# Performance work log

Hardware: AMD Instinct MI355X
Metric: run time of the kernel (lower is better)

## Reference

```python
import jax, jax.numpy as jnp
import numpy as np

N = 384      # max_nodes
H = 256      # layers[0] == layers[1] == layers[2]
Z = 128      # dim_z
ED = 128     # edge_dim
AH = ED // 2 # attention hidden

# complete directed graph: combinations (i<j) then reversed pairs
_i, _j = np.triu_indices(N, k=1)
_SRC = jnp.asarray(np.concatenate([_i, _j]), dtype=jnp.int32)  # edge_index[0]
_DST = jnp.asarray(np.concatenate([_j, _i]), dtype=jnp.int32)  # edge_index[1]


def setup_inputs() -> dict:
    key = jax.random.key(0)
    ks = jax.random.split(key, 16)
    def p(k, shape, fan_in):
        return jax.random.normal(k, shape, dtype=jnp.float32) * (1.0 / np.sqrt(fan_in))
    return {
        "z": jax.random.normal(ks[0], (1, Z), dtype=jnp.float32),
        # GRU (torch layout: W_ih [3H, Z], W_hh [3H, H]; gate order r, z, n)
        "gru_Wih": p(ks[1], (3 * H, Z), Z),
        "gru_Whh": p(ks[2], (3 * H, H), H),
        "gru_bih": jnp.zeros((3 * H,), jnp.float32),
        "gru_bhh": jnp.zeros((3 * H,), jnp.float32),
        # edge_generator MLP: 2H -> 4H -> ED
        "eg_W1": p(ks[3], (2 * H, 4 * H), 2 * H), "eg_b1": jnp.zeros((4 * H,), jnp.float32),
        "eg_W2": p(ks[4], (4 * H, ED), 4 * H),   "eg_b2": jnp.zeros((ED,), jnp.float32),
        # attention MLPs: (ED+H) -> ED//2 -> 1
        "att0_W1": p(ks[5], (ED + H, AH), ED + H), "att0_b1": jnp.zeros((AH,), jnp.float32),
        "att0_W2": p(ks[6], (AH, 1), AH),           "att0_b2": jnp.zeros((1,), jnp.float32),
        "att1_W1": p(ks[7], (ED + H, AH), ED + H), "att1_b1": jnp.zeros((AH,), jnp.float32),
        "att1_W2": p(ks[8], (AH, 1), AH),           "att1_b2": jnp.zeros((1,), jnp.float32),
        # EdgeConv output linears: H -> H
        "conv0_W": p(ks[9], (H, H), H),  "conv0_b": jnp.zeros((H,), jnp.float32),
        "conv1_W": p(ks[10], (H, H), H), "conv1_b": jnp.zeros((H,), jnp.float32),
    }


def _forward(z, gru_Wih, gru_Whh, gru_bih, gru_bhh,
             eg_W1, eg_b1, eg_W2, eg_b2,
             att0_W1, att0_b1, att0_W2, att0_b2,
             att1_W1, att1_b1, att1_W2, att1_b2,
             conv0_W, conv0_b, conv1_W, conv1_b):
    # --- GRU node generation: input is the same latent z at every step ---
    gi = z[0] @ gru_Wih.T + gru_bih            # [3H], constant per step
    gir, giz, gin = jnp.split(gi, 3)
    def step(h, _):
        gh = h @ gru_Whh.T + gru_bhh
        ghr, ghz, ghn = jnp.split(gh, 3)
        r = jax.nn.sigmoid(gir + ghr)
        u = jax.nn.sigmoid(giz + ghz)
        n = jnp.tanh(gin + r * ghn)
        h2 = (1.0 - u) * n + u * h
        return h2, h2
    _, nodes = jax.lax.scan(step, jnp.zeros((H,), z.dtype), None, length=N)  # [N, H]

    # --- edge features over the complete directed graph ---
    pairs = jnp.concatenate([nodes[_SRC], nodes[_DST]], axis=-1)            # [E, 2H]
    edges = jax.nn.relu(pairs @ eg_W1 + eg_b1) @ eg_W2 + eg_b2              # [E, ED]

    # --- EdgeConv: gather src, attention MLP gate, scatter-sum, linear ---
    def conv(x, aW1, ab1, aW2, ab2, W, b):
        xs = x[_SRC]                                                        # [E, H]
        a_in = jnp.concatenate([edges, xs], axis=-1)                        # [E, ED+H]
        att = jax.nn.sigmoid(jax.nn.relu(a_in @ aW1 + ab1) @ aW2 + ab2)     # [E, 1]
        agg = jax.ops.segment_sum(att * xs, _DST, num_segments=N)           # [N, H]
        return agg @ W + b

    x = jax.nn.relu(conv(nodes, att0_W1, att0_b1, att0_W2, att0_b2, conv0_W, conv0_b))
    x = conv(x, att1_W1, att1_b1, att1_W2, att1_b2, conv1_W, conv1_b)
    return jnp.sum(x, axis=0)                                               # [H]


def reference(z, gru_Wih, gru_Whh, gru_bih, gru_bhh,
              eg_W1, eg_b1, eg_W2, eg_b2,
              att0_W1, att0_b1, att0_W2, att0_b2,
              att1_W1, att1_b1, att1_W2, att1_b2,
              conv0_W, conv0_b, conv1_W, conv1_b):
    return _forward(z, gru_Wih, gru_Whh, gru_bih, gru_bhh,
                    eg_W1, eg_b1, eg_W2, eg_b2,
                    att0_W1, att0_b1, att0_W2, att0_b2,
                    att1_W1, att1_b1, att1_W2, att1_b2,
                    conv0_W, conv0_b, conv1_W, conv1_b)
```

## Files before the change

### kernel.cpp

```cpp
#include <hip/hip_runtime.h>
#include <hip/hip_fp16.h>
#include <cstdint>

#define DEV static __device__ __forceinline__

typedef _Float16 h2v __attribute__((ext_vector_type(2)));
typedef _Float16 half8 __attribute__((ext_vector_type(8)));
typedef float float4v __attribute__((ext_vector_type(4)));

union U32H2 { uint32_t u; _Float16 f[2]; };

DEV uint32_t pack_f2(float a, float b) {
    auto p = __builtin_amdgcn_cvt_pkrtz(a, b);
    return __builtin_bit_cast(uint32_t, p);
}

DEV half8 bc8(uint4 v) { return __builtin_bit_cast(half8, v); }

DEV float sigmoidf_(float x) { return 1.0f / (1.0f + __expf(-x)); }

DEV void gl_lds16(const void* gsrc, void* ldst) {
    __builtin_amdgcn_global_load_lds(
        (const __attribute__((address_space(1))) uint32_t*)gsrc,
        (__attribute__((address_space(3))) uint32_t*)ldst, 16, 0, 0);
}

DEV float pick4(float4v lo, float4v hi, int bsel, int r) {
    float v0 = bsel ? hi[0] : lo[0];
    float v1 = bsel ? hi[1] : lo[1];
    float v2 = bsel ? hi[2] : lo[2];
    float v3 = bsel ? hi[3] : lo[3];
    float x01 = (r & 1) ? v1 : v0;
    float x23 = (r & 1) ? v3 : v2;
    return (r & 2) ? x23 : x01;
}

static const size_t OFF_W16T  = 0;
static const size_t OFF_GI    = 98304;
static const size_t OFF_CC    = 99072;
static const size_t OFF_BF    = 99200;
static const size_t OFF_NODES = 164736;
static const size_t OFF_PF    = 263040;
static const size_t OFF_QF    = 459648;
static const size_t OFF_R0    = 656256;
static const size_t OFF_R1    = 680832;
static const size_t OFF_TT    = 705408;
static const size_t OFF_ATT0  = 10142592;
static const size_t OFF_ATT1  = 10290048;
static const size_t OFF_AGG   = 10437504;
static const size_t OFF_X0    = 10535808;
static const size_t OFF_CS    = 10634112;
static const size_t OFF_V     = 10634496;
static const size_t WS_TOTAL  = 10634752;

__global__ void k_prep_all(const float* __restrict__ Whh, uint32_t* __restrict__ WL,
                           const float* __restrict__ z, const float* __restrict__ Wih,
                           const float* __restrict__ bih, const float* __restrict__ bhh,
                           float* __restrict__ gs,
                           const float* __restrict__ egb2, const float* __restrict__ a0W1,
                           const float* __restrict__ a1W1, float* __restrict__ cc,
                           const float* __restrict__ egW2, uint32_t* __restrict__ BF) {
    int bb = blockIdx.x;
    if (bb < 96) {
        int o4 = bb * 256 + threadIdx.x;
        int c = o4 >> 9, t = o4 & 511;
        int rt = c >> 3, kt = c & 7;
        int lane = t & 63, wv = t >> 6;
        int row = (rt >> 1) * 256 + wv * 32 + ((rt & 1) << 4) + (lane & 15);
        int k0 = kt*32 + (lane >> 4)*8;
        const float* src = Whh + row*256 + k0;
        uint4 o;
        o.x = pack_f2(src[0], src[1]);
        o.y = pack_f2(src[2], src[3]);
        o.z = pack_f2(src[4], src[5]);
        o.w = pack_f2(src[6], src[7]);
        ((uint4*)WL)[o4] = o;
    } else if (bb < 99) {
        int o = (bb - 96) * 256 + threadIdx.x;
        float acc = bih[o];
        if (o < 512) acc += bhh[o];
        for (int i = 0; i < 128; ++i) acc += Wih[o*128 + i] * z[i];
        gs[o] = acc;
    } else if (bb == 99) {
        int t = threadIdx.x;
        if (t < 128) {
            const float* A = (t < 64) ? a0W1 : a1W1;
            int j = t & 63;
            float acc = 0.f;
            for (int i = 0; i < 128; ++i) acc += egb2[i] * A[i*64 + j];
            cc[t] = acc;
        }
    } else {
        int idx = (bb - 100) * 256 + threadIdx.x;
        int k2 = idx >> 7, n = idx & 127;
        const float* A = (n < 64) ? (a0W1 + n) : (a1W1 + (n - 64));
        const float* w0 = egW2 + (2*k2) * 128;
        float a = 0.f, b = 0.f;
        for (int i = 0; i < 128; ++i) {
            float av = A[i*64];
            a += w0[i] * av;
            b += w0[128 + i] * av;
        }
        int kk = k2 >> 4, jgrp = (k2 >> 2) & 3, sub = k2 & 3;
        int lane = jgrp*16 + (n & 15), t = n >> 4;
        BF[((kk*8 + t)*64 + lane)*4 + sub] = pack_f2(a, b);
    }
}

__global__ void __launch_bounds__(512, 2)
k_gru(const float* __restrict__ gs, const float* __restrict__ bhh,
      const uint32_t* __restrict__ WL, float* __restrict__ nodes) {
    int tid = threadIdx.x;
    int lane = tid & 63, wv = tid >> 6;
    int kq = lane >> 4, c = lane & 15;
    __shared__ __align__(16) _Float16 hh16[512];

    uint4 w[48];
    const uint4* wl4 = (const uint4*)WL;
    #pragma unroll
    for (int cc = 0; cc < 48; ++cc) w[cc] = wl4[cc*512 + tid];
    #pragma unroll
    for (int cc = 0; cc < 48; ++cc)
        asm volatile("" : "+a"(w[cc].x), "+a"(w[cc].y), "+a"(w[cc].z), "+a"(w[cc].w));

    const float L2E = 1.44269504088896f;
    int r = c & 3, bsel = (c >> 2) & 1;
    int i_loc = kq*4 + r + bsel*16;
    int gidx = wv*32 + i_loc;
    float pr = -L2E * gs[gidx];
    float pz = -L2E * gs[256 + gidx];
    float gin_l = gs[512 + gidx];
    float bn_l  = bhh[512 + gidx];
    float pn = -2.f * L2E * gin_l;
    bool active = (c < 8);

    float h = 0.f;
    if (tid < 256) ((uint32_t*)hh16)[tid] = 0u;
    __syncthreads();

    const float4v z4 = {0.f, 0.f, 0.f, 0.f};
    int par = 0;
    for (int t = 0; t < 384; ++t) {
        const _Float16* hb = hh16 + par*256 + kq*8;
        uint4 b[8];
        #pragma unroll
        for (int kt = 0; kt < 8; ++kt) b[kt] = *(const uint4*)(hb + kt*32);

        float4v d0, d1, d2, d3, d4, d5;
        d0 = __builtin_amdgcn_mfma_f32_16x16x32_f16(bc8(w[0]),  bc8(b[0]), z4, 0, 0, 0);
        d1 = __builtin_amdgcn_mfma_f32_16x16x32_f16(bc8(w[8]),  bc8(b[0]), z4, 0, 0, 0);
        #pragma unroll
        for (int kt = 1; kt < 8; ++kt) {
            d0 = __builtin_amdgcn_mfma_f32_16x16x32_f16(bc8(w[kt]),    bc8(b[kt]), d0, 0, 0, 0);
            d1 = __builtin_amdgcn_mfma_f32_16x16x32_f16(bc8(w[8+kt]),  bc8(b[kt]), d1, 0, 0, 0);
        }
        float ghr = pick4(d0, d1, bsel, r);
        float er = __builtin_amdgcn_exp2f(__builtin_fmaf(ghr, -L2E, pr));
        float rg = __builtin_amdgcn_rcpf(1.f + er);

        d2 = __builtin_amdgcn_mfma_f32_16x16x32_f16(bc8(w[16]), bc8(b[0]), z4, 0, 0, 0);
        d3 = __builtin_amdgcn_mfma_f32_16x16x32_f16(bc8(w[24]), bc8(b[0]), z4, 0, 0, 0);
        d4 = __builtin_amdgcn_mfma_f32_16x16x32_f16(bc8(w[32]), bc8(b[0]), z4, 0, 0, 0);
        d5 = __builtin_amdgcn_mfma_f32_16x16x32_f16(bc8(w[40]), bc8(b[0]), z4, 0, 0, 0);
        #pragma unroll
        for (int kt = 1; kt < 8; ++kt) {
            d2 = __builtin_amdgcn_mfma_f32_16x16x32_f16(bc8(w[16+kt]), bc8(b[kt]), d2, 0, 0, 0);
            d3 = __builtin_amdgcn_mfma_f32_16x16x32_f16(bc8(w[24+kt]), bc8(b[kt]), d3, 0, 0, 0);
            d4 = __builtin_amdgcn_mfma_f32_16x16x32_f16(bc8(w[32+kt]), bc8(b[kt]), d4, 0, 0, 0);
            d5 = __builtin_amdgcn_mfma_f32_16x16x32_f16(bc8(w[40+kt]), bc8(b[kt]), d5, 0, 0, 0);
        }

        float ghz = pick4(d2, d3, bsel, r);
        float ghn = pick4(d4, d5, bsel, r);
        float eu = __builtin_amdgcn_exp2f(__builtin_fmaf(ghz, -L2E, pz));
        float u  = __builtin_amdgcn_rcpf(1.f + eu);
        float tm = ghn + bn_l;
        float q  = __builtin_fmaf(rg * tm, -2.f * L2E, pn);
        float e2 = __builtin_amdgcn_exp2f(q);
        float nn = __builtin_fmaf(2.f, __builtin_amdgcn_rcpf(1.f + e2), -1.f);
        h = nn + u * (h - nn);

        if (active) {
            hh16[(par ^ 1)*256 + gidx] = (_Float16)h;
            nodes[t*256 + gidx] = h;
        }
        asm volatile("s_waitcnt lgkmcnt(0)" ::: "memory");
        __builtin_amdgcn_sched_barrier(0);
        __builtin_amdgcn_s_barrier();
        __builtin_amdgcn_sched_barrier(0);
        par ^= 1;
    }
}

__global__ void k_pq(const float* __restrict__ nodes, const float* __restrict__ eg_W1,
                     const float* __restrict__ eg_b1, const float* __restrict__ a0W1,
                     const float* __restrict__ a0b1, const float* __restrict__ cc,
                     uint32_t* __restrict__ PF, uint32_t* __restrict__ QF,
                     float* __restrict__ R0) {
    int tid = threadIdx.x;
    int s0 = blockIdx.x * 4;
    __shared__ float ns[4][256];
    #pragma unroll
    for (int q = 0; q < 4; ++q) ns[q][tid] = nodes[(s0+q)*256 + tid];
    __syncthreads();

    int k0 = tid * 4;
    float acc[4][4];
    #pragma unroll
    for (int q = 0; q < 4; ++q) { acc[q][0]=0;acc[q][1]=0;acc[q][2]=0;acc[q][3]=0; }
    for (int i = 0; i < 256; ++i) {
        float4 wv = *(const float4*)&eg_W1[i*1024 + k0];
        #pragma unroll
        for (int q = 0; q < 4; ++q) {
            float nv = ns[q][i];
            acc[q][0] += nv*wv.x; acc[q][1] += nv*wv.y;
            acc[q][2] += nv*wv.z; acc[q][3] += nv*wv.w;
        }
    }
    float4 bv = *(const float4*)&eg_b1[k0];
    {
        int kk = k0 >> 5;
        int lgrp = ((k0 >> 3) & 3) * 16;
        int sub = (k0 & 7) >> 1;
        #pragma unroll
        for (int q = 0; q < 4; ++q) {
            int s = s0 + q, g = s >> 4, srow = s & 15;
            uint2 pw;
            pw.x = pack_f2(acc[q][0] + bv.x, acc[q][1] + bv.y);
            pw.y = pack_f2(acc[q][2] + bv.z, acc[q][3] + bv.w);
            *(uint2*)(PF + (((g*32 + kk)*64 + lgrp + srow) << 2) + sub) = pw;
        }
    }

    #pragma unroll
    for (int q = 0; q < 4; ++q) { acc[q][0]=0;acc[q][1]=0;acc[q][2]=0;acc[q][3]=0; }
    for (int i = 0; i < 256; ++i) {
        float4 wv = *(const float4*)&eg_W1[(256+i)*1024 + k0];
        #pragma unroll
        for (int q = 0; q < 4; ++q) {
            float nv = ns[q][i];
            acc[q][0] += nv*wv.x; acc[q][1] += nv*wv.y;
            acc[q][2] += nv*wv.z; acc[q][3] += nv*wv.w;
        }
    }
    #pragma unroll
    for (int q = 0; q < 4; ++q) {
        uint2 pw;
        pw.x = pack_f2(acc[q][0], acc[q][1]);
        pw.y = pack_f2(acc[q][2], acc[q][3]);
        ((uint2*)QF)[(s0+q)*256 + tid] = pw;
    }

    int srow = tid >> 6, j = tid & 63;
    float racc = a0b1[j] + cc[j];
    for (int i = 0; i < 256; ++i) racc += ns[srow][i] * a0W1[(128+i)*64 + j];
    R0[(s0+srow)*64 + j] = racc;
}

DEV void stageA(const uint32_t* __restrict__ PF, const uint32_t* __restrict__ BF,
                int g, int hc, char* buf, int tid) {
    const char* psrc = (const char*)(PF + ((size_t)g*32 + (size_t)hc*2) * 256);
    if (tid < 128) gl_lds16(psrc + tid*16, buf + tid*16);
    const char* bsrc = (const char*)(BF + (size_t)hc * 4096);
    #pragma unroll
    for (int i = 0; i < 4; ++i)
        gl_lds16(bsrc + tid*16 + i*4096, buf + 2048 + tid*16 + i*4096);
}

__global__ void __launch_bounds__(256, 2)
k_phaseA_mfma(const uint32_t* __restrict__ PF, const uint32_t* __restrict__ QF,
              const uint32_t* __restrict__ BF, uint32_t* __restrict__ TT) {
    __shared__ __align__(16) char smem[69632];
    uint4* Qs4 = (uint4*)smem;
    char* bufbase = smem + 32768;

    int tid = threadIdx.x;
    int lane = tid & 63, wv = tid >> 6;
    int g = blockIdx.x, d0 = blockIdx.y * 16;

    {
        const char* src = (const char*)(QF + (size_t)d0 * 512);
        int off = tid * 16;
        #pragma unroll
        for (int i = 0; i < 8; ++i)
            gl_lds16(src + off + i*4096, (char*)Qs4 + off + i*4096);
    }
    stageA(PF, BF, g, 0, bufbase, tid);
    asm volatile("s_waitcnt vmcnt(0)" ::: "memory");
    __builtin_amdgcn_sched_barrier(0);
    __builtin_amdgcn_s_barrier();
    __builtin_amdgcn_sched_barrier(0);

    float4v acc[4][8];
    #pragma unroll
    for (int t = 0; t < 4; ++t)
        #pragma unroll
        for (int n = 0; n < 8; ++n) acc[t][n] = 0.f;

    for (int hc = 0; hc < 16; ++hc) {
        char* cur = bufbase + (hc & 1) * 18432;
        char* nxt = bufbase + ((hc + 1) & 1) * 18432;
        if (hc < 15) stageA(PF, BF, g, hc + 1, nxt, tid);

        uint4* Ph = (uint4*)cur;
        uint4* Bh = (uint4*)(cur + 2048);
        #pragma unroll
        for (int kkl = 0; kkl < 2; ++kkl) {
            int kkg = hc*2 + kkl;
            half8 b[8];
            #pragma unroll
            for (int n = 0; n < 8; ++n) b[n] = bc8(Bh[(kkl*8 + n)*64 + lane]);
            half8 p8 = bc8(Ph[kkl*64 + lane]);
            #pragma unroll
            for (int t = 0; t < 4; ++t) {
                half8 q8 = bc8(Qs4[(wv*4 + t)*128 + kkg*4 + (lane >> 4)]);
                half8 x = p8 + q8;
                half8 zz = 0;
                x = __builtin_elementwise_max(x, zz);
                #pragma unroll
                for (int n = 0; n < 8; ++n)
                    acc[t][n] = __builtin_amdgcn_mfma_f32_16x16x32_f16(x, b[n], acc[t][n], 0, 0, 0);
            }
        }
        asm volatile("s_waitcnt vmcnt(0)" ::: "memory");
        __builtin_amdgcn_sched_barrier(0);
        __builtin_amdgcn_s_barrier();
        __builtin_amdgcn_sched_barrier(0);
    }

    _Float16* epi = (_Float16*)(smem + 32768);
    int cn = lane & 15, rhi = (lane >> 4) * 4;
    for (int half = 0; half < 2; ++half) {
        __syncthreads();
        #pragma unroll
        for (int t = 0; t < 4; ++t) {
            int dl = wv*4 + t;
            #pragma unroll
            for (int n = 0; n < 4; ++n) {
                int j = n*16 + cn;
                float4v v = acc[t][half*4 + n];
                #pragma unroll
                for (int r = 0; r < 4; ++r)
                    epi[((rhi + r)*16 + dl)*64 + j] = (_Float16)v[r];
            }
        }
        __syncthreads();
        int srow = tid >> 4, dl = tid & 15;
        const uint4* src = (const uint4*)(epi + tid*64);
        uint4* dst = (uint4*)(TT + ((size_t)((g*16 + srow)*384 + d0 + dl))*64 + half*32);
        #pragma unroll
        for (int q = 0; q < 8; ++q) dst[q] = src[q];
    }
}

__global__ void k_att(const uint32_t* __restrict__ TT, const float* __restrict__ R,
                      const float* __restrict__ w2, const float* __restrict__ b2,
                      int off, float* __restrict__ ATT, float* __restrict__ CS) {
    int tid = threadIdx.x;
    int p = blockIdx.x * 256 + tid;
    int s = p / 384, d = p - s * 384;
    int sa = (blockIdx.x * 256) / 384;
    __shared__ float w2s[64];
    __shared__ float rs[2][64];
    if (tid < 64) w2s[tid] = w2[tid];
    else if (tid < 128) rs[0][tid - 64] = R[sa*64 + (tid - 64)];
    else if (tid < 192) {
        int sb = sa + 1;
        rs[1][tid - 128] = (sb < 384) ? R[sb*64 + (tid - 128)] : 0.f;
    }
    __syncthreads();
    const uint4* tp = (const uint4*)(TT + (size_t)p*64 + off);
    const float* rp = (s == sa) ? rs[0] : rs[1];
    float logit = b2[0];
    #pragma unroll
    for (int m = 0; m < 8; ++m) {
        uint4 tv = tp[m];
        uint32_t us[4] = {tv.x, tv.y, tv.z, tv.w};
        #pragma unroll
        for (int q = 0; q < 4; ++q) {
            U32H2 c; c.u = us[q];
            int j = m*8 + q*2;
            float h0 = fmaxf((float)c.f[0] + rp[j],   0.f);
            float h1 = fmaxf((float)c.f[1] + rp[j+1], 0.f);
            logit += h0*w2s[j] + h1*w2s[j+1];
        }
    }
    float a = 1.f / (1.f + __expf(-logit));
    float a_eff = (s == d) ? 0.f : a;
    ATT[p] = a_eff;

    if (CS) {
        float va = (s == sa) ? a_eff : 0.f;
        float vb = (s != sa) ? a_eff : 0.f;
        #pragma unroll
        for (int o = 32; o > 0; o >>= 1) {
            va += __shfl_down(va, o, 64);
            vb += __shfl_down(vb, o, 64);
        }
        if ((tid & 63) == 0) {
            atomicAdd(&CS[sa], va);
            int sb = sa + 1;
            if (sb < 384) atomicAdd(&CS[sb], vb);
        }
    }
}

__global__ void __launch_bounds__(256)
k_agg(const float* __restrict__ ATT, const float* __restrict__ X,
      float* __restrict__ AGG) {
    int tid = threadIdx.x;
    int d0 = blockIdx.x * 16;
    __shared__ float att_s[16][17];
    float acc[16];
    #pragma unroll
    for (int dl = 0; dl < 16; ++dl) acc[dl] = 0.f;

    for (int s0 = 0; s0 < 384; s0 += 16) {
        __syncthreads();
        {
            int row = tid >> 4, col = tid & 15;
            att_s[row][col] = ATT[(s0 + row)*384 + d0 + col];
        }
        __syncthreads();
        #pragma unroll 4
        for (int ss = 0; ss < 16; ++ss) {
            float x = X[(s0 + ss)*256 + tid];
            #pragma unroll
            for (int dl = 0; dl < 16; ++dl) acc[dl] += att_s[ss][dl] * x;
        }
    }
    #pragma unroll
    for (int dl = 0; dl < 16; ++dl)
        AGG[(d0 + dl)*256 + tid] = acc[dl];
}

__global__ void k_x0r1(const float* __restrict__ AGG, const float* __restrict__ W,
                       const float* __restrict__ b, const float* __restrict__ a1W1,
                       const float* __restrict__ a1b1, const float* __restrict__ cc,
                       float* __restrict__ X0, float* __restrict__ R1) {
    int d = blockIdx.x, tid = threadIdx.x;
    __shared__ float ag[256];
    __shared__ float xs[256];
    ag[tid] = AGG[d*256 + tid];
    __syncthreads();
    float acc = b[tid];
    for (int i = 0; i < 256; ++i) acc += ag[i] * W[i*256 + tid];
    acc = fmaxf(acc, 0.f);
    X0[d*256 + tid] = acc;
    xs[tid] = acc;
    __syncthreads();
    if (tid < 64) {
        float r = a1b1[tid] + cc[64 + tid];
        for (int i = 0; i < 256; ++i) r += xs[i] * a1W1[(128+i)*64 + tid];
        R1[d*64 + tid] = r;
    }
}

__global__ void k_vout(const float* __restrict__ CS, const float* __restrict__ X0,
                       const float* __restrict__ W, const float* __restrict__ b,
                       float* __restrict__ out) {
    int tid = threadIdx.x;
    __shared__ float cs[384];
    __shared__ float vs[256];
    for (int q = tid; q < 384; q += 256) cs[q] = CS[q];
    __syncthreads();
    float acc = 0.f;
    for (int s = 0; s < 384; s += 4) {
        acc += cs[s]*X0[s*256 + tid] + cs[s+1]*X0[(s+1)*256 + tid]
             + cs[s+2]*X0[(s+2)*256 + tid] + cs[s+3]*X0[(s+3)*256 + tid];
    }
    vs[tid] = acc;
    __syncthreads();
    float o = 384.f * b[tid];
    for (int i = 0; i < 256; ++i) o += vs[i] * W[i*256 + tid];
    out[tid] = o;
}

extern "C" void kernel_launch(void* const* d_in, const int* in_sizes, int n_in,
                              void* d_out, int out_size, void* d_ws, size_t ws_size,
                              hipStream_t stream) {
    if (ws_size < WS_TOTAL * sizeof(uint32_t)) return;

    const float* z    = (const float*)d_in[0];
    const float* Wih  = (const float*)d_in[1];
    const float* Whh  = (const float*)d_in[2];
    const float* bih  = (const float*)d_in[3];
    const float* bhh  = (const float*)d_in[4];
    const float* egW1 = (const float*)d_in[5];
    const float* egb1 = (const float*)d_in[6];
    const float* egW2 = (const float*)d_in[7];
    const float* egb2 = (const float*)d_in[8];
    const float* a0W1 = (const float*)d_in[9];
    const float* a0b1 = (const float*)d_in[10];
    const float* a0W2 = (const float*)d_in[11];
    const float* a0b2 = (const float*)d_in[12];
    const float* a1W1 = (const float*)d_in[13];
    const float* a1b1 = (const float*)d_in[14];
    const float* a1W2 = (const float*)d_in[15];
    const float* a1b2 = (const float*)d_in[16];
    const float* c0W  = (const float*)d_in[17];
    const float* c0b  = (const float*)d_in[18];
    const float* c1W  = (const float*)d_in[19];
    const float* c1b  = (const float*)d_in[20];

    uint32_t* ws   = (uint32_t*)d_ws;
    uint32_t* WL   = ws + OFF_W16T;
    float*    gi   = (float*)(ws + OFF_GI);
    float*    cc   = (float*)(ws + OFF_CC);
    uint32_t* BF   = ws + OFF_BF;
    float*    nodes= (float*)(ws + OFF_NODES);
    uint32_t* PF   = ws + OFF_PF;
    uint32_t* QF   = ws + OFF_QF;
    float*    R0   = (float*)(ws + OFF_R0);
    float*    R1   = (float*)(ws + OFF_R1);
    uint32_t* TT   = ws + OFF_TT;
    float*    ATT0 = (float*)(ws + OFF_ATT0);
    float*    ATT1 = (float*)(ws + OFF_ATT1);
    float*    AGG  = (float*)(ws + OFF_AGG);
    float*    X0   = (float*)(ws + OFF_X0);
    float*    CS   = (float*)(ws + OFF_CS);
    float*    out  = (float*)d_out;

    hipMemsetAsync(CS, 0, 384 * sizeof(float), stream);
    hipLaunchKernelGGL(k_prep_all,    dim3(356), dim3(256), 0, stream,
                       Whh, WL, z, Wih, bih, bhh, gi, egb2, a0W1, a1W1, cc, egW2, BF);
    hipLaunchKernelGGL(k_gru,         dim3(1),   dim3(512), 0, stream, gi, bhh, WL, nodes);
    hipLaunchKernelGGL(k_pq,          dim3(96),  dim3(256), 0, stream, nodes, egW1, egb1, a0W1, a0b1, cc, PF, QF, R0);
    hipLaunchKernelGGL(k_phaseA_mfma, dim3(24, 24), dim3(256), 0, stream, PF, QF, BF, TT);
    hipLaunchKernelGGL(k_att,         dim3(576), dim3(256), 0, stream, TT, R0, a0W2, a0b2, 0,  ATT0, (float*)nullptr);
    hipLaunchKernelGGL(k_agg,         dim3(24),  dim3(256), 0, stream, ATT0, nodes, AGG);
    hipLaunchKernelGGL(k_x0r1,        dim3(384), dim3(256), 0, stream, AGG, c0W, c0b, a1W1, a1b1, cc, X0, R1);
    hipLaunchKernelGGL(k_att,         dim3(576), dim3(256), 0, stream, TT, R1, a1W2, a1b2, 32, ATT1, CS);
    hipLaunchKernelGGL(k_vout,        dim3(1),   dim3(256), 0, stream, CS, X0, c1W, c1b, out);
}
```

Before: 699.5 us.

## Fuse prep, GRU, PQ, edge MLP and first attention into persistent ticketed megakernel

Merges the prep, GRU, node projection, edge-MLP MFMA and first attention kernels into one launch. Blocks take work items from an atomic ticket counter and wait on global flags. The GRU block publishes node progress every 16 steps, so the projection and edge tiles can start while the serial recurrence is still running instead of after it finishes. The first attention logit is computed in the edge-tile epilogue, which removes a separate pass over TT. The cost is spin-wait traffic, tiles that depend on late nodes stalling, and a reliance on ticket ordering to avoid deadlock.

```diff
diff --git a/kernel.cpp b/kernel.cpp
--- a/kernel.cpp
+++ b/kernel.cpp
@@ -16,8 +16,6 @@
 }
 
 DEV half8 bc8(uint4 v) { return __builtin_bit_cast(half8, v); }
-
-DEV float sigmoidf_(float x) { return 1.0f / (1.0f + __expf(-x)); }
 
 DEV void gl_lds16(const void* gsrc, void* ldst) {
     __builtin_amdgcn_global_load_lds(
@@ -33,6 +31,18 @@
     float x01 = (r & 1) ? v1 : v0;
     float x23 = (r & 1) ? v3 : v2;
     return (r & 2) ? x23 : x01;
+}
+
+DEV uint32_t aload_acq(const uint32_t* p) {
+    return __hip_atomic_load(p, __ATOMIC_ACQUIRE, __HIP_MEMORY_SCOPE_AGENT);
+}
+DEV void spin_eq(const uint32_t* p, uint32_t v) {
+    int cap = 1 << 27;
+    while (aload_acq(p) != v && --cap) __builtin_amdgcn_s_sleep(16);
+}
+DEV void spin_ge(const uint32_t* p, uint32_t v) {
+    int cap = 1 << 27;
+    while (aload_acq(p) < v && --cap) __builtin_amdgcn_s_sleep(16);
 }
 
 static const size_t OFF_W16T  = 0;
@@ -51,19 +61,32 @@
 static const size_t OFF_X0    = 10535808;
 static const size_t OFF_CS    = 10634112;
 static const size_t OFF_V     = 10634496;
-static const size_t WS_TOTAL  = 10634752;
-
-__global__ void k_prep_all(const float* __restrict__ Whh, uint32_t* __restrict__ WL,
-                           const float* __restrict__ z, const float* __restrict__ Wih,
-                           const float* __restrict__ bih, const float* __restrict__ bhh,
-                           float* __restrict__ gs,
-                           const float* __restrict__ egb2, const float* __restrict__ a0W1,
-                           const float* __restrict__ a1W1, float* __restrict__ cc,
-                           const float* __restrict__ egW2, uint32_t* __restrict__ BF) {
-    int bb = blockIdx.x;
-    if (bb < 96) {
-        int o4 = bb * 256 + threadIdx.x;
-        int c = o4 >> 9, t = o4 & 511;
+static const size_t OFF_CNT   = 10634752;
+static const size_t WS_TOTAL  = 10634816;
+
+__global__ void __launch_bounds__(512, 2)
+k_mega(const float* __restrict__ Whh, const float* __restrict__ z,
+       const float* __restrict__ Wih, const float* __restrict__ bih,
+       const float* __restrict__ bhh,
+       const float* __restrict__ egW1, const float* __restrict__ egb1,
+       const float* __restrict__ egW2, const float* __restrict__ egb2,
+       const float* __restrict__ a0W1, const float* __restrict__ a0b1,
+       const float* __restrict__ a0W2, const float* __restrict__ a0b2,
+       const float* __restrict__ a1W1,
+       uint32_t* __restrict__ WL, float* __restrict__ cc,
+       uint32_t* __restrict__ BF, float* __restrict__ nodes,
+       uint32_t* __restrict__ PF, uint32_t* __restrict__ QF,
+       float* __restrict__ R0, uint32_t* __restrict__ TT,
+       float* __restrict__ ATT0, uint32_t* __restrict__ cnt) {
+    __shared__ __align__(16) char smem[69632];
+    __shared__ int ticket_s;
+    int tid = threadIdx.x;
+    if (tid == 0) ticket_s = (int)atomicAdd(&cnt[0], 1u);
+    __syncthreads();
+    int ticket = ticket_s;
+
+    if (ticket < 48) {
+        int c = ticket, t = tid;
         int rt = c >> 3, kt = c & 7;
         int lane = t & 63, wv = t >> 6;
         int row = (rt >> 1) * 256 + wv * 32 + ((rt & 1) << 4) + (lane & 15);
@@ -74,24 +97,131 @@
         o.y = pack_f2(src[2], src[3]);
         o.z = pack_f2(src[4], src[5]);
         o.w = pack_f2(src[6], src[7]);
-        ((uint4*)WL)[o4] = o;
-    } else if (bb < 99) {
-        int o = (bb - 96) * 256 + threadIdx.x;
-        float acc = bih[o];
-        if (o < 512) acc += bhh[o];
-        for (int i = 0; i < 128; ++i) acc += Wih[o*128 + i] * z[i];
-        gs[o] = acc;
-    } else if (bb == 99) {
-        int t = threadIdx.x;
-        if (t < 128) {
-            const float* A = (t < 64) ? a0W1 : a1W1;
-            int j = t & 63;
+        ((uint4*)WL)[c*512 + t] = o;
+        __threadfence();
+        __syncthreads();
+        if (tid == 0)
+            __hip_atomic_fetch_add(&cnt[1], 1u, __ATOMIC_RELEASE, __HIP_MEMORY_SCOPE_AGENT);
+    } else if (ticket == 48) {
+        _Float16* hh16 = (_Float16*)smem;
+        float* zs = (float*)(smem + 1024);
+        int lane = tid & 63, wv = tid >> 6;
+        int kq = lane >> 4, c = lane & 15;
+        const float L2E = 1.44269504088896f;
+        int r = c & 3, bsel = (c >> 2) & 1;
+        int gidx = wv*32 + kq*4 + r + bsel*16;
+        bool active = (c < 8);
+
+        if (tid < 128) zs[tid] = z[tid];
+        if (tid < 256) ((uint32_t*)hh16)[tid] = 0u;
+        __syncthreads();
+
+        float s_r = bih[gidx] + bhh[gidx];
+        float s_z = bih[256 + gidx] + bhh[256 + gidx];
+        float s_n = bih[512 + gidx];
+        {
+            const float4* wr = (const float4*)(Wih + (size_t)gidx*128);
+            const float4* wzp = (const float4*)(Wih + (size_t)(256+gidx)*128);
+            const float4* wn = (const float4*)(Wih + (size_t)(512+gidx)*128);
+            for (int i = 0; i < 32; ++i) {
+                float4 zv = ((const float4*)zs)[i];
+                float4 a = wr[i], b = wzp[i], d = wn[i];
+                s_r += a.x*zv.x + a.y*zv.y + a.z*zv.z + a.w*zv.w;
+                s_z += b.x*zv.x + b.y*zv.y + b.z*zv.z + b.w*zv.w;
+                s_n += d.x*zv.x + d.y*zv.y + d.z*zv.z + d.w*zv.w;
+            }
+        }
+        float pr = -L2E * s_r;
+        float pz = -L2E * s_z;
+        float pn = -2.f * L2E * s_n;
+        float bn_l = bhh[512 + gidx];
+
+        spin_eq(&cnt[1], 48);
+
+        uint4 w[48];
+        const uint4* wl4 = (const uint4*)WL;
+        #pragma unroll
+        for (int q = 0; q < 48; ++q) w[q] = wl4[q*512 + tid];
+        #pragma unroll
+        for (int q = 0; q < 48; ++q)
+            asm volatile("" : "+a"(w[q].x), "+a"(w[q].y), "+a"(w[q].z), "+a"(w[q].w));
+
+        float h = 0.f;
+        __syncthreads();
+        const float4v z4 = {0.f, 0.f, 0.f, 0.f};
+        int par = 0;
+        for (int t = 0; t < 384; ++t) {
+            const _Float16* hb = hh16 + par*256 + kq*8;
+            uint4 b[8];
+            #pragma unroll
+            for (int kt = 0; kt < 8; ++kt) b[kt] = *(const uint4*)(hb + kt*32);
+
+            float4v d0, d1, d2, d3, d4, d5;
+            d0 = __builtin_amdgcn_mfma_f32_16x16x32_f16(bc8(w[0]),  bc8(b[0]), z4, 0, 0, 0);
+            d1 = __builtin_amdgcn_mfma_f32_16x16x32_f16(bc8(w[8]),  bc8(b[0]), z4, 0, 0, 0);
+            #pragma unroll
+            for (int kt = 1; kt < 8; ++kt) {
+                d0 = __builtin_amdgcn_mfma_f32_16x16x32_f16(bc8(w[kt]),   bc8(b[kt]), d0, 0, 0, 0);
+                d1 = __builtin_amdgcn_mfma_f32_16x16x32_f16(bc8(w[8+kt]), bc8(b[kt]), d1, 0, 0, 0);
+            }
+            float ghr = pick4(d0, d1, bsel, r);
+            float er = __builtin_amdgcn_exp2f(__builtin_fmaf(ghr, -L2E, pr));
+            float rg = __builtin_amdgcn_rcpf(1.f + er);
+
+            d2 = __builtin_amdgcn_mfma_f32_16x16x32_f16(bc8(w[16]), bc8(b[0]), z4, 0, 0, 0);
+            d3 = __builtin_amdgcn_mfma_f32_16x16x32_f16(bc8(w[24]), bc8(b[0]), z4, 0, 0, 0);
+            d4 = __builtin_amdgcn_mfma_f32_16x16x32_f16(bc8(w[32]), bc8(b[0]), z4, 0, 0, 0);
+            d5 = __builtin_amdgcn_mfma_f32_16x16x32_f16(bc8(w[40]), bc8(b[0]), z4, 0, 0, 0);
+            #pragma unroll
+            for (int kt = 1; kt < 8; ++kt) {
+                d2 = __builtin_amdgcn_mfma_f32_16x16x32_f16(bc8(w[16+kt]), bc8(b[kt]), d2, 0, 0, 0);
+                d3 = __builtin_amdgcn_mfma_f32_16x16x32_f16(bc8(w[24+kt]), bc8(b[kt]), d3, 0, 0, 0);
+                d4 = __builtin_amdgcn_mfma_f32_16x16x32_f16(bc8(w[32+kt]), bc8(b[kt]), d4, 0, 0, 0);
+                d5 = __builtin_amdgcn_mfma_f32_16x16x32_f16(bc8(w[40+kt]), bc8(b[kt]), d5, 0, 0, 0);
+            }
+
+            float ghz = pick4(d2, d3, bsel, r);
+            float ghn = pick4(d4, d5, bsel, r);
+            float eu = __builtin_amdgcn_exp2f(__builtin_fmaf(ghz, -L2E, pz));
+            float u  = __builtin_amdgcn_rcpf(1.f + eu);
+            float tm = ghn + bn_l;
+            float q  = __builtin_fmaf(rg * tm, -2.f * L2E, pn);
+            float e2 = __builtin_amdgcn_exp2f(q);
+            float nn = __builtin_fmaf(2.f, __builtin_amdgcn_rcpf(1.f + e2), -1.f);
+            h = nn + u * (h - nn);
+
+            if (active) {
+                hh16[(par ^ 1)*256 + gidx] = (_Float16)h;
+                nodes[t*256 + gidx] = h;
+            }
+            bool pub = (t & 15) == 15;
+            if (pub) __threadfence();
+            asm volatile("s_waitcnt lgkmcnt(0)" ::: "memory");
+            __builtin_amdgcn_sched_barrier(0);
+            __builtin_amdgcn_s_barrier();
+            __builtin_amdgcn_sched_barrier(0);
+            if (pub && tid == 0)
+                __hip_atomic_store(&cnt[4], (uint32_t)(t+1), __ATOMIC_RELEASE, __HIP_MEMORY_SCOPE_AGENT);
+            par ^= 1;
+        }
+        __threadfence();
+        __syncthreads();
+        if (tid == 0)
+            __hip_atomic_store(&cnt[4], 384u, __ATOMIC_RELEASE, __HIP_MEMORY_SCOPE_AGENT);
+    } else if (ticket == 49) {
+        if (tid < 128) {
+            const float* A = (tid < 64) ? a0W1 : a1W1;
+            int j = tid & 63;
             float acc = 0.f;
             for (int i = 0; i < 128; ++i) acc += egb2[i] * A[i*64 + j];
-            cc[t] = acc;
-        }
-    } else {
-        int idx = (bb - 100) * 256 + threadIdx.x;
+            cc[tid] = acc;
+        }
+        __threadfence();
+        __syncthreads();
+        if (tid == 0)
+            __hip_atomic_store(&cnt[2], 1u, __ATOMIC_RELEASE, __HIP_MEMORY_SCOPE_AGENT);
+    } else if (ticket < 178) {
+        int idx = (ticket - 50) * 512 + tid;
         int k2 = idx >> 7, n = idx & 127;
         const float* A = (n < 64) ? (a0W1 + n) : (a1W1 + (n - 64));
         const float* w0 = egW2 + (2*k2) * 128;
@@ -104,252 +234,195 @@
         int kk = k2 >> 4, jgrp = (k2 >> 2) & 3, sub = k2 & 3;
         int lane = jgrp*16 + (n & 15), t = n >> 4;
         BF[((kk*8 + t)*64 + lane)*4 + sub] = pack_f2(a, b);
-    }
-}
-
-__global__ void __launch_bounds__(512, 2)
-k_gru(const float* __restrict__ gs, const float* __restrict__ bhh,
-      const uint32_t* __restrict__ WL, float* __restrict__ nodes) {
-    int tid = threadIdx.x;
-    int lane = tid & 63, wv = tid >> 6;
-    int kq = lane >> 4, c = lane & 15;
-    __shared__ __align__(16) _Float16 hh16[512];
-
-    uint4 w[48];
-    const uint4* wl4 = (const uint4*)WL;
-    #pragma unroll
-    for (int cc = 0; cc < 48; ++cc) w[cc] = wl4[cc*512 + tid];
-    #pragma unroll
-    for (int cc = 0; cc < 48; ++cc)
-        asm volatile("" : "+a"(w[cc].x), "+a"(w[cc].y), "+a"(w[cc].z), "+a"(w[cc].w));
-
-    const float L2E = 1.44269504088896f;
-    int r = c & 3, bsel = (c >> 2) & 1;
-    int i_loc = kq*4 + r + bsel*16;
-    int gidx = wv*32 + i_loc;
-    float pr = -L2E * gs[gidx];
-    float pz = -L2E * gs[256 + gidx];
-    float gin_l = gs[512 + gidx];
-    float bn_l  = bhh[512 + gidx];
-    float pn = -2.f * L2E * gin_l;
-    bool active = (c < 8);
-
-    float h = 0.f;
-    if (tid < 256) ((uint32_t*)hh16)[tid] = 0u;
-    __syncthreads();
-
-    const float4v z4 = {0.f, 0.f, 0.f, 0.f};
-    int par = 0;
-    for (int t = 0; t < 384; ++t) {
-        const _Float16* hb = hh16 + par*256 + kq*8;
-        uint4 b[8];
+        __threadfence();
+        __syncthreads();
+        if (tid == 0)
+            __hip_atomic_fetch_add(&cnt[3], 1u, __ATOMIC_RELEASE, __HIP_MEMORY_SCOPE_AGENT);
+    } else if (ticket < 226) {
+        int k = ticket - 178;
+        int s0 = k * 8;
+        float* ns = (float*)smem;
+        spin_eq(&cnt[2], 1);
+        spin_ge(&cnt[4], (uint32_t)(s0 + 8));
+        for (int i = tid; i < 2048; i += 512)
+            ns[i] = nodes[(size_t)s0*256 + i];
+        __syncthreads();
+
+        int tp = tid & 255;
+        int k0 = tp * 4;
+        bool isQ = tid >= 256;
+        float acc[8][4];
         #pragma unroll
-        for (int kt = 0; kt < 8; ++kt) b[kt] = *(const uint4*)(hb + kt*32);
-
-        float4v d0, d1, d2, d3, d4, d5;
-        d0 = __builtin_amdgcn_mfma_f32_16x16x32_f16(bc8(w[0]),  bc8(b[0]), z4, 0, 0, 0);
-        d1 = __builtin_amdgcn_mfma_f32_16x16x32_f16(bc8(w[8]),  bc8(b[0]), z4, 0, 0, 0);
-        #pragma unroll
-        for (int kt = 1; kt < 8; ++kt) {
-            d0 = __builtin_amdgcn_mfma_f32_16x16x32_f16(bc8(w[kt]),    bc8(b[kt]), d0, 0, 0, 0);
-            d1 = __builtin_amdgcn_mfma_f32_16x16x32_f16(bc8(w[8+kt]),  bc8(b[kt]), d1, 0, 0, 0);
-        }
-        float ghr = pick4(d0, d1, bsel, r);
-        float er = __builtin_amdgcn_exp2f(__builtin_fmaf(ghr, -L2E, pr));
-        float rg = __builtin_amdgcn_rcpf(1.f + er);
-
-        d2 = __builtin_amdgcn_mfma_f32_16x16x32_f16(bc8(w[16]), bc8(b[0]), z4, 0, 0, 0);
-        d3 = __builtin_amdgcn_mfma_f32_16x16x32_f16(bc8(w[24]), bc8(b[0]), z4, 0, 0, 0);
-        d4 = __builtin_amdgcn_mfma_f32_16x16x32_f16(bc8(w[32]), bc8(b[0]), z4, 0, 0, 0);
-        d5 = __builtin_amdgcn_mfma_f32_16x16x32_f16(bc8(w[40]), bc8(b[0]), z4, 0, 0, 0);
-        #pragma unroll
-        for (int kt = 1; kt < 8; ++kt) {
-            d2 = __builtin_amdgcn_mfma_f32_16x16x32_f16(bc8(w[16+kt]), bc8(b[kt]), d2, 0, 0, 0);
-            d3 = __builtin_amdgcn_mfma_f32_16x16x32_f16(bc8(w[24+kt]), bc8(b[kt]), d3, 0, 0, 0);
-            d4 = __builtin_amdgcn_mfma_f32_16x16x32_f16(bc8(w[32+kt]), bc8(b[kt]), d4, 0, 0, 0);
-            d5 = __builtin_amdgcn_mfma_f32_16x16x32_f16(bc8(w[40+kt]), bc8(b[kt]), d5, 0, 0, 0);
-        }
-
-        float ghz = pick4(d2, d3, bsel, r);
-        float ghn = pick4(d4, d5, bsel, r);
-        float eu = __builtin_amdgcn_exp2f(__builtin_fmaf(ghz, -L2E, pz));
-        float u  = __builtin_amdgcn_rcpf(1.f + eu);
-        float tm = ghn + bn_l;
-        float q  = __builtin_fmaf(rg * tm, -2.f * L2E, pn);
-        float e2 = __builtin_amdgcn_exp2f(q);
-        float nn = __builtin_fmaf(2.f, __builtin_amdgcn_rcpf(1.f + e2), -1.f);
-        h = nn + u * (h - nn);
-
-        if (active) {
-            hh16[(par ^ 1)*256 + gidx] = (_Float16)h;
-            nodes[t*256 + gidx] = h;
-        }
-        asm volatile("s_waitcnt lgkmcnt(0)" ::: "memory");
-        __builtin_amdgcn_sched_barrier(0);
-        __builtin_amdgcn_s_barrier();
-        __builtin_amdgcn_sched_barrier(0);
-        par ^= 1;
-    }
-}
-
-__global__ void k_pq(const float* __restrict__ nodes, const float* __restrict__ eg_W1,
-                     const float* __restrict__ eg_b1, const float* __restrict__ a0W1,
-                     const float* __restrict__ a0b1, const float* __restrict__ cc,
-                     uint32_t* __restrict__ PF, uint32_t* __restrict__ QF,
-                     float* __restrict__ R0) {
-    int tid = threadIdx.x;
-    int s0 = blockIdx.x * 4;
-    __shared__ float ns[4][256];
-    #pragma unroll
-    for (int q = 0; q < 4; ++q) ns[q][tid] = nodes[(s0+q)*256 + tid];
-    __syncthreads();
-
-    int k0 = tid * 4;
-    float acc[4][4];
-    #pragma unroll
-    for (int q = 0; q < 4; ++q) { acc[q][0]=0;acc[q][1]=0;acc[q][2]=0;acc[q][3]=0; }
-    for (int i = 0; i < 256; ++i) {
-        float4 wv = *(const float4*)&eg_W1[i*1024 + k0];
-        #pragma unroll
-        for (int q = 0; q < 4; ++q) {
-            float nv = ns[q][i];
-            acc[q][0] += nv*wv.x; acc[q][1] += nv*wv.y;
-            acc[q][2] += nv*wv.z; acc[q][3] += nv*wv.w;
-        }
-    }
-    float4 bv = *(const float4*)&eg_b1[k0];
-    {
-        int kk = k0 >> 5;
-        int lgrp = ((k0 >> 3) & 3) * 16;
-        int sub = (k0 & 7) >> 1;
-        #pragma unroll
-        for (int q = 0; q < 4; ++q) {
-            int s = s0 + q, g = s >> 4, srow = s & 15;
-            uint2 pw;
-            pw.x = pack_f2(acc[q][0] + bv.x, acc[q][1] + bv.y);
-            pw.y = pack_f2(acc[q][2] + bv.z, acc[q][3] + bv.w);
-            *(uint2*)(PF + (((g*32 + kk)*64 + lgrp + srow) << 2) + sub) = pw;
-        }
-    }
-
-    #pragma unroll
-    for (int q = 0; q < 4; ++q) { acc[q][0]=0;acc[q][1]=0;acc[q][2]=0;acc[q][3]=0; }
-    for (int i = 0; i < 256; ++i) {
-        float4 wv = *(const float4*)&eg_W1[(256+i)*1024 + k0];
-        #pragma unroll
-        for (int q = 0; q < 4; ++q) {
-            float nv = ns[q][i];
-            acc[q][0] += nv*wv.x; acc[q][1] += nv*wv.y;
-            acc[q][2] += nv*wv.z; acc[q][3] += nv*wv.w;
-        }
-    }
-    #pragma unroll
-    for (int q = 0; q < 4; ++q) {
-        uint2 pw;
-        pw.x = pack_f2(acc[q][0], acc[q][1]);
-        pw.y = pack_f2(acc[q][2], acc[q][3]);
-        ((uint2*)QF)[(s0+q)*256 + tid] = pw;
-    }
-
-    int srow = tid >> 6, j = tid & 63;
-    float racc = a0b1[j] + cc[j];
-    for (int i = 0; i < 256; ++i) racc += ns[srow][i] * a0W1[(128+i)*64 + j];
-    R0[(s0+srow)*64 + j] = racc;
-}
-
-DEV void stageA(const uint32_t* __restrict__ PF, const uint32_t* __restrict__ BF,
-                int g, int hc, char* buf, int tid) {
-    const char* psrc = (const char*)(PF + ((size_t)g*32 + (size_t)hc*2) * 256);
-    if (tid < 128) gl_lds16(psrc + tid*16, buf + tid*16);
-    const char* bsrc = (const char*)(BF + (size_t)hc * 4096);
-    #pragma unroll
-    for (int i = 0; i < 4; ++i)
-        gl_lds16(bsrc + tid*16 + i*4096, buf + 2048 + tid*16 + i*4096);
-}
-
-__global__ void __launch_bounds__(256, 2)
-k_phaseA_mfma(const uint32_t* __restrict__ PF, const uint32_t* __restrict__ QF,
-              const uint32_t* __restrict__ BF, uint32_t* __restrict__ TT) {
-    __shared__ __align__(16) char smem[69632];
-    uint4* Qs4 = (uint4*)smem;
-    char* bufbase = smem + 32768;
-
-    int tid = threadIdx.x;
-    int lane = tid & 63, wv = tid >> 6;
-    int g = blockIdx.x, d0 = blockIdx.y * 16;
-
-    {
-        const char* src = (const char*)(QF + (size_t)d0 * 512);
-        int off = tid * 16;
-        #pragma unroll
-        for (int i = 0; i < 8; ++i)
-            gl_lds16(src + off + i*4096, (char*)Qs4 + off + i*4096);
-    }
-    stageA(PF, BF, g, 0, bufbase, tid);
-    asm volatile("s_waitcnt vmcnt(0)" ::: "memory");
-    __builtin_amdgcn_sched_barrier(0);
-    __builtin_amdgcn_s_barrier();
-    __builtin_amdgcn_sched_barrier(0);
-
-    float4v acc[4][8];
-    #pragma unroll
-    for (int t = 0; t < 4; ++t)
-        #pragma unroll
-        for (int n = 0; n < 8; ++n) acc[t][n] = 0.f;
-
-    for (int hc = 0; hc < 16; ++hc) {
-        char* cur = bufbase + (hc & 1) * 18432;
-        char* nxt = bufbase + ((hc + 1) & 1) * 18432;
-        if (hc < 15) stageA(PF, BF, g, hc + 1, nxt, tid);
-
-        uint4* Ph = (uint4*)cur;
-        uint4* Bh = (uint4*)(cur + 2048);
-        #pragma unroll
-        for (int kkl = 0; kkl < 2; ++kkl) {
-            int kkg = hc*2 + kkl;
-            half8 b[8];
-            #pragma unroll
-            for (int n = 0; n < 8; ++n) b[n] = bc8(Bh[(kkl*8 + n)*64 + lane]);
-            half8 p8 = bc8(Ph[kkl*64 + lane]);
-            #pragma unroll
-            for (int t = 0; t < 4; ++t) {
-                half8 q8 = bc8(Qs4[(wv*4 + t)*128 + kkg*4 + (lane >> 4)]);
-                half8 x = p8 + q8;
-                half8 zz = 0;
-                x = __builtin_elementwise_max(x, zz);
-                #pragma unroll
-                for (int n = 0; n < 8; ++n)
-                    acc[t][n] = __builtin_amdgcn_mfma_f32_16x16x32_f16(x, b[n], acc[t][n], 0, 0, 0);
-            }
+        for (int q = 0; q < 8; ++q) { acc[q][0]=0;acc[q][1]=0;acc[q][2]=0;acc[q][3]=0; }
+        const float* Wbase = egW1 + (isQ ? (size_t)256*1024 : 0) + k0;
+        for (int i = 0; i < 256; ++i) {
+            float4 wv = *(const float4*)&Wbase[(size_t)i*1024];
+            #pragma unroll
+            for (int q = 0; q < 8; ++q) {
+                float nv = ns[q*256 + i];
+                acc[q][0] += nv*wv.x; acc[q][1] += nv*wv.y;
+                acc[q][2] += nv*wv.z; acc[q][3] += nv*wv.w;
+            }
+        }
+        if (!isQ) {
+            float4 bv = *(const float4*)&egb1[k0];
+            int kk = k0 >> 5;
+            int lgrp = ((k0 >> 3) & 3) * 16;
+            int sub = (k0 & 7) >> 1;
+            #pragma unroll
+            for (int q = 0; q < 8; ++q) {
+                int s = s0 + q, g = s >> 4, srow = s & 15;
+                uint2 pw;
+                pw.x = pack_f2(acc[q][0] + bv.x, acc[q][1] + bv.y);
+                pw.y = pack_f2(acc[q][2] + bv.z, acc[q][3] + bv.w);
+                *(uint2*)(PF + (((g*32 + kk)*64 + lgrp + srow) << 2) + sub) = pw;
+            }
+        } else {
+            #pragma unroll
+            for (int q = 0; q < 8; ++q) {
+                uint2 pw;
+                pw.x = pack_f2(acc[q][0], acc[q][1]);
+                pw.y = pack_f2(acc[q][2], acc[q][3]);
+                ((uint2*)QF)[(size_t)(s0+q)*256 + tp] = pw;
+            }
+        }
+        {
+            int srow = tid >> 6, j = tid & 63;
+            float racc = a0b1[j] + cc[j];
+            for (int i = 0; i < 256; ++i) racc += ns[srow*256 + i] * a0W1[(128+i)*64 + j];
+            R0[(s0+srow)*64 + j] = racc;
+        }
+        __threadfence();
+        __syncthreads();
+        if (tid == 0)
+            __hip_atomic_store(&cnt[8 + k], 1u, __ATOMIC_RELEASE, __HIP_MEMORY_SCOPE_AGENT);
+    } else {
+        int id = ticket - 226;
+        int m = (int)__builtin_sqrtf((float)id + 0.5f);
+        while (m*m > id) --m;
+        while ((m+1)*(m+1) <= id) ++m;
+        int rem = id - m*m;
+        int g, dt;
+        if (rem <= m) { g = m; dt = rem; } else { g = rem - m - 1; dt = m; }
+        int d0 = dt * 16;
+
+        spin_eq(&cnt[3], 128);
+        spin_eq(&cnt[8 + 2*g], 1);
+        spin_eq(&cnt[8 + 2*g + 1], 1);
+        spin_eq(&cnt[8 + 2*dt], 1);
+        spin_eq(&cnt[8 + 2*dt + 1], 1);
+
+        uint4* Qs4 = (uint4*)smem;
+        char* bufbase = smem + 32768;
+        int lane = tid & 63, wv = tid >> 6;
+
+        {
+            const char* src = (const char*)(QF + (size_t)d0 * 512);
+            for (int off = tid*16; off < 32768; off += 8192)
+                gl_lds16(src + off, (char*)Qs4 + off);
+        }
+        {
+            const char* psrc = (const char*)(PF + (size_t)g * 8192);
+            if (tid < 128) gl_lds16(psrc + tid*16, bufbase + tid*16);
+            const char* bsrc = (const char*)BF;
+            #pragma unroll
+            for (int i = 0; i < 2; ++i)
+                gl_lds16(bsrc + tid*16 + i*8192, bufbase + 2048 + tid*16 + i*8192);
         }
         asm volatile("s_waitcnt vmcnt(0)" ::: "memory");
         __builtin_amdgcn_sched_barrier(0);
         __builtin_amdgcn_s_barrier();
         __builtin_amdgcn_sched_barrier(0);
-    }
-
-    _Float16* epi = (_Float16*)(smem + 32768);
-    int cn = lane & 15, rhi = (lane >> 4) * 4;
-    for (int half = 0; half < 2; ++half) {
-        __syncthreads();
+
+        float4v acc[2][8];
         #pragma unroll
-        for (int t = 0; t < 4; ++t) {
-            int dl = wv*4 + t;
-            #pragma unroll
-            for (int n = 0; n < 4; ++n) {
-                int j = n*16 + cn;
-                float4v v = acc[t][half*4 + n];
+        for (int t = 0; t < 2; ++t)
+            #pragma unroll
+            for (int n = 0; n < 8; ++n) acc[t][n] = 0.f;
+
+        for (int hc = 0; hc < 16; ++hc) {
+            char* cur = bufbase + (hc & 1) * 18432;
+            char* nxt = bufbase + ((hc + 1) & 1) * 18432;
+            if (hc < 15) {
+                const char* psrc = (const char*)(PF + ((size_t)g*32 + (size_t)(hc+1)*2) * 256);
+                if (tid < 128) gl_lds16(psrc + tid*16, nxt + tid*16);
+                const char* bsrc = (const char*)(BF + (size_t)(hc+1) * 4096);
                 #pragma unroll
-                for (int r = 0; r < 4; ++r)
-                    epi[((rhi + r)*16 + dl)*64 + j] = (_Float16)v[r];
-            }
-        }
-        __syncthreads();
-        int srow = tid >> 4, dl = tid & 15;
-        const uint4* src = (const uint4*)(epi + tid*64);
-        uint4* dst = (uint4*)(TT + ((size_t)((g*16 + srow)*384 + d0 + dl))*64 + half*32);
-        #pragma unroll
-        for (int q = 0; q < 8; ++q) dst[q] = src[q];
+                for (int i = 0; i < 2; ++i)
+                    gl_lds16(bsrc + tid*16 + i*8192, nxt + 2048 + tid*16 + i*8192);
+            }
+            uint4* Ph = (uint4*)cur;
+            uint4* Bh = (uint4*)(cur + 2048);
+            #pragma unroll
+            for (int kkl = 0; kkl < 2; ++kkl) {
+                int kkg = hc*2 + kkl;
+                half8 b[8];
+                #pragma unroll
+                for (int n = 0; n < 8; ++n) b[n] = bc8(Bh[(kkl*8 + n)*64 + lane]);
+                half8 p8 = bc8(Ph[kkl*64 + lane]);
+                #pragma unroll
+                for (int t = 0; t < 2; ++t) {
+                    half8 q8 = bc8(Qs4[(wv*2 + t)*128 + kkg*4 + (lane >> 4)]);
+                    half8 x = p8 + q8;
+                    half8 zz = 0;
+                    x = __builtin_elementwise_max(x, zz);
+                    #pragma unroll
+                    for (int n = 0; n < 8; ++n)
+                        acc[t][n] = __builtin_amdgcn_mfma_f32_16x16x32_f16(x, b[n], acc[t][n], 0, 0, 0);
+                }
+            }
+            asm volatile("s_waitcnt vmcnt(0)" ::: "memory");
+            __builtin_amdgcn_sched_barrier(0);
+            __builtin_amdgcn_s_barrier();
+            __builtin_amdgcn_sched_barrier(0);
+        }
+
+        __syncthreads();
+        float* R0s = (float*)smem;
+        float* w2s = (float*)(smem + 4096);
+        for (int i = tid; i < 1024; i += 512)
+            R0s[i] = R0[(size_t)(g*16 + (i >> 6))*64 + (i & 63)];
+        if (tid < 64) w2s[tid] = a0W2[tid];
+        float b2v = a0b2[0];
+
+        _Float16* epi = (_Float16*)(smem + 32768);
+        int cn = lane & 15, rhi = (lane >> 4) * 4;
+        for (int half = 0; half < 2; ++half) {
+            __syncthreads();
+            #pragma unroll
+            for (int t = 0; t < 2; ++t) {
+                int dl = wv*2 + t;
+                #pragma unroll
+                for (int n = 0; n < 4; ++n) {
+                    int j = n*16 + cn;
+                    float4v v = acc[t][half*4 + n];
+                    #pragma unroll
+                    for (int r = 0; r < 4; ++r)
+                        epi[((rhi + r)*16 + dl)*64 + j] = (_Float16)v[r];
+                }
+            }
+            __syncthreads();
+            {
+                int p = tid >> 1, sub = tid & 1;
+                int srow = p >> 4, dl = p & 15;
+                const uint4* src = (const uint4*)(epi + (size_t)p*64);
+                uint4* dst = (uint4*)(TT + ((size_t)((g*16 + srow)*384 + d0 + dl))*64 + half*32);
+                #pragma unroll
+                for (int q = 0; q < 4; ++q) dst[sub*4 + q] = src[sub*4 + q];
+            }
+            if (half == 0 && tid < 256) {
+                int sl = tid >> 4, dl = tid & 15;
+                const _Float16* tp = epi + (size_t)(sl*16 + dl)*64;
+                const float* rp = R0s + sl*64;
+                float logit = b2v;
+                #pragma unroll
+                for (int j = 0; j < 64; ++j)
+                    logit += fmaxf((float)tp[j] + rp[j], 0.f) * w2s[j];
+                float a = 1.f / (1.f + __expf(-logit));
+                int s = g*16 + sl, d = d0 + dl;
+                ATT0[(size_t)s*384 + d] = (s == d) ? 0.f : a;
+            }
+        }
     }
 }
 
@@ -505,7 +578,6 @@
 
     uint32_t* ws   = (uint32_t*)d_ws;
     uint32_t* WL   = ws + OFF_W16T;
-    float*    gi   = (float*)(ws + OFF_GI);
     float*    cc   = (float*)(ws + OFF_CC);
     uint32_t* BF   = ws + OFF_BF;
     float*    nodes= (float*)(ws + OFF_NODES);
@@ -519,17 +591,16 @@
     float*    AGG  = (float*)(ws + OFF_AGG);
     float*    X0   = (float*)(ws + OFF_X0);
     float*    CS   = (float*)(ws + OFF_CS);
+    uint32_t* cnt  = ws + OFF_CNT;
     float*    out  = (float*)d_out;
 
-    hipMemsetAsync(CS, 0, 384 * sizeof(float), stream);
-    hipLaunchKernelGGL(k_prep_all,    dim3(356), dim3(256), 0, stream,
-                       Whh, WL, z, Wih, bih, bhh, gi, egb2, a0W1, a1W1, cc, egW2, BF);
-    hipLaunchKernelGGL(k_gru,         dim3(1),   dim3(512), 0, stream, gi, bhh, WL, nodes);
-    hipLaunchKernelGGL(k_pq,          dim3(96),  dim3(256), 0, stream, nodes, egW1, egb1, a0W1, a0b1, cc, PF, QF, R0);
-    hipLaunchKernelGGL(k_phaseA_mfma, dim3(24, 24), dim3(256), 0, stream, PF, QF, BF, TT);
-    hipLaunchKernelGGL(k_att,         dim3(576), dim3(256), 0, stream, TT, R0, a0W2, a0b2, 0,  ATT0, (float*)nullptr);
-    hipLaunchKernelGGL(k_agg,         dim3(24),  dim3(256), 0, stream, ATT0, nodes, AGG);
-    hipLaunchKernelGGL(k_x0r1,        dim3(384), dim3(256), 0, stream, AGG, c0W, c0b, a1W1, a1b1, cc, X0, R1);
-    hipLaunchKernelGGL(k_att,         dim3(576), dim3(256), 0, stream, TT, R1, a1W2, a1b2, 32, ATT1, CS);
-    hipLaunchKernelGGL(k_vout,        dim3(1),   dim3(256), 0, stream, CS, X0, c1W, c1b, out);
-}
+    hipMemsetAsync(CS, 0, (WS_TOTAL - OFF_CS) * sizeof(uint32_t), stream);
+    hipLaunchKernelGGL(k_mega, dim3(802), dim3(512), 0, stream,
+                       Whh, z, Wih, bih, bhh, egW1, egb1, egW2, egb2,
+                       a0W1, a0b1, a0W2, a0b2, a1W1,
+                       WL, cc, BF, nodes, PF, QF, R0, TT, ATT0, cnt);
+    hipLaunchKernelGGL(k_agg,  dim3(24),  dim3(256), 0, stream, ATT0, nodes, AGG);
+    hipLaunchKernelGGL(k_x0r1, dim3(384), dim3(256), 0, stream, AGG, c0W, c0b, a1W1, a1b1, cc, X0, R1);
+    hipLaunchKernelGGL(k_att,  dim3(576), dim3(256), 0, stream, TT, R1, a1W2, a1b2, 32, ATT1, CS);
+    hipLaunchKernelGGL(k_vout, dim3(1),   dim3(256), 0, stream, CS, X0, c1W, c1b, out);
+}
```

New measurement: 2.009 ms. +187.2%, slower.
